# Optimization experiments

Hardware: AMD Instinct MI355X
Metric: run time of the kernel (lower is better)

## Reference

```python
import jax, jax.numpy as jnp
import numpy as np

B, L, DIN, DQ, DS, DP = 16, 2048, 1024, 128, 64, 32

def _lin(k, din, dout):
    k1, k2 = jax.random.split(k)
    s = 1.0 / np.sqrt(din)
    W = jax.random.uniform(k1, (din, dout), jnp.float32, -s, s)
    b = jax.random.uniform(k2, (dout,), jnp.float32, -s, s)
    return W, b

def setup_inputs() -> dict:
    key = jax.random.key(0)
    ks = jax.random.split(key, 13)
    Wq, bq = _lin(ks[0], DIN, DQ)
    Wk, bk = _lin(ks[1], DIN, DQ)
    Wv, bv = _lin(ks[2], DIN, DQ)
    W1, b1 = _lin(ks[3], DS + DP, 128)
    W2, b2 = _lin(ks[4], 128, DQ)
    Wqc, bqc = _lin(ks[5], DQ, DQ)
    Wkc, bkc = _lin(ks[6], DQ, DQ)
    return dict(
        query=jax.random.normal(ks[7], (B, L, DIN), jnp.float32),
        key=jax.random.normal(ks[8], (B, L, DIN), jnp.float32),
        value=jax.random.normal(ks[9], (B, L, DIN), jnp.float32),
        sf=jax.random.normal(ks[10], (B, DS), jnp.float32),
        pos=jax.random.normal(ks[11], (L, DP), jnp.float32),
        Wq=Wq, bq=bq, Wk=Wk, bk=bk, Wv=Wv, bv=bv,
        W1=W1, b1=b1, W2=W2, b2=b2,
        Wqc=Wqc, bqc=bqc, Wkc=Wkc, bkc=bkc,
    )

def reference(query, key, value, sf, pos,
              Wq, bq, Wk, bk, Wv, bv,
              W1, b1, W2, b2, Wqc, bqc, Wkc, bkc):
    b, l, _ = query.shape
    q = query @ Wq + bq            # [b, l, dq]
    k = key @ Wk + bk              # [b, l, dq]
    v = value @ Wv + bv            # [b, l, dq]
    # CPE bias branch (pos is not None)
    sf_exp = jnp.broadcast_to(sf[:, None, :], (b, l, sf.shape[1]))
    pos_exp = jnp.broadcast_to(pos[None, :, :], (b, l, pos.shape[1]))
    cpe = jnp.concatenate([sf_exp, pos_exp], axis=2)         # [b, l, ds+32]
    cpe = jax.nn.relu(cpe @ W1 + b1) @ W2 + b2               # [b, l, dq]
    qc = cpe @ Wqc + bqc
    kc = cpe @ Wkc + bkc
    bias = jnp.einsum('bld,bmd->blm', qc, kc)                # [b, l, l]
    # add_mode == 0: post-softmax additive bias
    scale = jnp.sqrt(jnp.asarray(q.shape[-1], q.dtype))
    scores = jnp.einsum('bld,bmd->blm', q, k) / scale
    attn = jax.nn.softmax(scores, axis=-1) + bias
    out = jnp.einsum('blm,bmd->bld', attn, v)
    # L1 diff-norm regularizer over bias (use_cls=False)
    norm3 = (jnp.sum(jnp.abs(bias[:, 1:, :] - bias[:, :-1, :])) +
             jnp.sum(jnp.abs(bias[:, :, 1:] - bias[:, :, :-1])))
    return out, norm3
```

## Files before the change

### kernel.cpp

```cpp
#include <hip/hip_runtime.h>
#include <hip/hip_bf16.h>

typedef __attribute__((ext_vector_type(8))) short short8;
typedef __attribute__((ext_vector_type(4))) short short4x;
typedef __attribute__((ext_vector_type(4))) float floatx4;

#define MFMA16(a,b,c) __builtin_amdgcn_mfma_f32_16x16x32_bf16((a),(b),(c),0,0,0)

__device__ __forceinline__ unsigned short f2bf(float f) {
  unsigned int x = __float_as_uint(f);
  return (unsigned short)((x + 0x7fffu + ((x >> 16) & 1u)) >> 16);
}
__device__ __forceinline__ float bf2f(unsigned short s) {
  return __uint_as_float(((unsigned int)s) << 16);
}
__device__ __forceinline__ unsigned short f2bf_cvt(float f) {
  unsigned int r;
  asm("v_cvt_pk_bf16_f32 %0, %1, %1" : "=v"(r) : "v"(f));
  return (unsigned short)r;
}

__global__ __launch_bounds__(256)
void prep_kernel(const float* __restrict__ Wq, const float* __restrict__ Wk,
                 const float* __restrict__ Wv, const float* __restrict__ W1,
                 const float* __restrict__ b1, const float* __restrict__ W2,
                 const float* __restrict__ b2, const float* __restrict__ Wqc,
                 const float* __restrict__ bqc, const float* __restrict__ Wkc,
                 const float* __restrict__ bkc, const float* __restrict__ sf,
                 const float* __restrict__ pos,
                 unsigned short* __restrict__ Wf, unsigned short* __restrict__ Ut,
                 float* __restrict__ cqck, float* __restrict__ Asf,
                 float* __restrict__ Ppos)
{
  int blk = blockIdx.x, t = threadIdx.x;
  if (blk < 24) {
    int mat = blk >> 3, cg = blk & 7;
    const float* W = (mat == 0) ? Wq : (mat == 1) ? Wk : Wv;
    int l = t & 63, jp = t >> 6;
    int col = cg * 16 + (l & 15);
    unsigned short* o = Wf + (size_t)mat * 131072 + (size_t)cg * 32 * 512 + l * 8 + jp * 2;
    for (int ks = 0; ks < 32; ++ks) {
      int k = ks * 32 + (l >> 4) * 8 + jp * 2;
      o[ks * 512 + 0] = f2bf(W[(size_t)k * 128 + col]);
      o[ks * 512 + 1] = f2bf(W[(size_t)(k + 1) * 128 + col]);
    }
  } else if (blk >= 384 && blk < 512) {
    int j = blk - 384;
    int k = t & 127;
    const float* Wc = (t < 128) ? Wqc : Wkc;
    float acc = 0.f;
    for (int h = 0; h < 128; ++h) acc += W2[k * 128 + h] * Wc[h * 128 + j];
    Ut[(size_t)((t < 128) ? j : 128 + j) * 128 + k] = f2bf(acc);
  } else if (blk == 512) {
    int j = t & 127;
    const float* Wc = (t < 128) ? Wqc : Wkc;
    const float* bc = (t < 128) ? bqc : bkc;
    float acc = bc[j];
    for (int k = 0; k < 128; ++k) acc += b2[k] * Wc[k * 128 + j];
    cqck[t] = acc;
  } else if (blk > 512 && blk < 529) {
    int b = blk - 513;
    if (t < 128) {
      float acc = 0.f;
      for (int i = 0; i < 64; ++i) acc += sf[b * 64 + i] * W1[i * 128 + t];
      Asf[b * 128 + t] = acc;
    }
  } else if (blk >= 529) {
    int l = blk - 529;
    if (t < 128) {
      float acc = b1[t];
      for (int i = 0; i < 32; ++i) acc += pos[l * 32 + i] * W1[(64 + i) * 128 + t];
      Ppos[l * 128 + t] = acc;
    }
  }
}

__global__ __launch_bounds__(256)
void proj_kernel(const float* __restrict__ X, const unsigned short* __restrict__ Wf,
                 const float* __restrict__ bias,
                 unsigned short* __restrict__ qo, unsigned short* __restrict__ ko,
                 unsigned short* __restrict__ vto, int which)
{
  __shared__ __align__(16) unsigned short X_lds[32 * 1032];

  int t = threadIdx.x;
  int w = t >> 6, l = t & 63;
  int rowbase = blockIdx.x * 32;
  const int lrow = l & 15, hi = l >> 4;
  const float RS2 = 0.08838834764831845f * 1.4426950408889634f;

#pragma unroll
  for (int r = 0; r < 8; ++r) {
    int row = w * 8 + r;
    const float* src = X + (size_t)(rowbase + row) * 1024 + l * 4;
    unsigned short* dst = &X_lds[row * 1032 + l * 4];
#pragma unroll
    for (int i = 0; i < 4; ++i) {
      float4 v = *(const float4*)(src + i * 256);
      short4x s;
      s[0] = (short)f2bf(v.x); s[1] = (short)f2bf(v.y);
      s[2] = (short)f2bf(v.z); s[3] = (short)f2bf(v.w);
      *(short4x*)(dst + i * 256) = s;
    }
  }
  __syncthreads();

  const unsigned short* wp0 = Wf + (size_t)(w * 2) * 32 * 512 + l * 8;
  const unsigned short* wp1 = Wf + (size_t)(w * 2 + 1) * 32 * 512 + l * 8;
  const int xo0 = lrow * 1032 + hi * 8;
  const int xo1 = (lrow + 16) * 1032 + hi * 8;

  floatx4 acc[2][2];
#pragma unroll
  for (int i = 0; i < 2; ++i)
#pragma unroll
    for (int j = 0; j < 2; ++j) { acc[i][j][0]=0.f; acc[i][j][1]=0.f; acc[i][j][2]=0.f; acc[i][j][3]=0.f; }

#pragma unroll 4
  for (int ks = 0; ks < 32; ++ks) {
    short8 b0 = *(const short8*)(wp0 + ks * 512);
    short8 b1 = *(const short8*)(wp1 + ks * 512);
    short8 a0 = *(const short8*)&X_lds[xo0 + ks * 32];
    short8 a1 = *(const short8*)&X_lds[xo1 + ks * 32];
    acc[0][0] = MFMA16(a0, b0, acc[0][0]);
    acc[0][1] = MFMA16(a0, b1, acc[0][1]);
    acc[1][0] = MFMA16(a1, b0, acc[1][0]);
    acc[1][1] = MFMA16(a1, b1, acc[1][1]);
  }

#pragma unroll
  for (int mf = 0; mf < 2; ++mf)
#pragma unroll
    for (int nf = 0; nf < 2; ++nf) {
      int col = w * 32 + nf * 16 + lrow;
      float bb = bias[col];
#pragma unroll
      for (int j = 0; j < 4; ++j) {
        int grow = rowbase + mf * 16 + hi * 4 + j;
        float v = acc[mf][nf][j] + bb;
        if (which == 0) qo[(size_t)grow * 128 + col] = f2bf(v * RS2);
        else if (which == 1) ko[(size_t)grow * 128 + col] = f2bf(v);
        else {
          int b = grow >> 11, li = grow & 2047;
          vto[((size_t)b * 128 + col) * 2048 + li] = f2bf(v);
        }
      }
    }
}

__global__ __launch_bounds__(256)
void qckc_kernel(const float* __restrict__ Asf, const float* __restrict__ Ppos,
                 const unsigned short* __restrict__ Ut, const float* __restrict__ cqck,
                 unsigned short* __restrict__ qc, unsigned short* __restrict__ kc)
{
  __shared__ __align__(16) unsigned short hid[64 * 136];
  int t = threadIdx.x, w = t >> 6, l = t & 63;
  int lbase = blockIdx.x * 64;
  int b = lbase >> 11;
  const int lrow = l & 15, lk = (l >> 4) * 8;
  {
    int r = t >> 2, seg = (t & 3) * 32;
    const float* pp = Ppos + (size_t)((lbase + r) & 2047) * 128 + seg;
    const float* aa = Asf + b * 128 + seg;
    unsigned short* dst = hid + r * 136 + seg;
#pragma unroll
    for (int c = 0; c < 32; c += 4) {
      float4 p4 = *(const float4*)(pp + c);
      float4 a4 = *(const float4*)(aa + c);
      dst[c + 0] = f2bf(fmaxf(p4.x + a4.x, 0.f));
      dst[c + 1] = f2bf(fmaxf(p4.y + a4.y, 0.f));
      dst[c + 2] = f2bf(fmaxf(p4.z + a4.z, 0.f));
      dst[c + 3] = f2bf(fmaxf(p4.w + a4.w, 0.f));
    }
  }
  __syncthreads();
  short8 a[4];
#pragma unroll
  for (int ks = 0; ks < 4; ++ks)
    a[ks] = *(const short8*)&hid[(w * 16 + lrow) * 136 + ks * 32 + lk];
  floatx4 acc[16];
#pragma unroll
  for (int nf = 0; nf < 16; ++nf) { acc[nf][0]=0.f; acc[nf][1]=0.f; acc[nf][2]=0.f; acc[nf][3]=0.f; }
#pragma unroll
  for (int nf = 0; nf < 16; ++nf)
#pragma unroll
    for (int ks = 0; ks < 4; ++ks) {
      short8 bfr = *(const short8*)(Ut + (size_t)(nf * 16 + lrow) * 128 + ks * 32 + lk);
      acc[nf] = MFMA16(a[ks], bfr, acc[nf]);
    }
#pragma unroll
  for (int nf = 0; nf < 16; ++nf) {
    int col = nf * 16 + lrow;
    float bb = cqck[col];
#pragma unroll
    for (int j = 0; j < 4; ++j) {
      int grow = lbase + w * 16 + (l >> 4) * 4 + j;
      float v = acc[nf][j] + bb;
      if (col < 128) qc[(size_t)grow * 128 + col] = f2bf(v);
      else kc[(size_t)grow * 128 + (col - 128)] = f2bf(v);
    }
  }
}

__global__ __launch_bounds__(256)
void m2_partial_kernel(const unsigned short* __restrict__ vt,
                       const unsigned short* __restrict__ kc,
                       float* __restrict__ M2p)
{
  __shared__ __align__(16) unsigned short kct[128 * 40];
  int ks = blockIdx.x, b = blockIdx.y;
  int t = threadIdx.x, w = t >> 6, l = t & 63;
  const int lrow = l & 15, lk = (l >> 4) * 8;
  floatx4 acc[2][8];
#pragma unroll
  for (int i = 0; i < 2; ++i)
#pragma unroll
    for (int j = 0; j < 8; ++j) { acc[i][j][0]=0.f; acc[i][j][1]=0.f; acc[i][j][2]=0.f; acc[i][j][3]=0.f; }
  for (int mc = 0; mc < 8; ++mc) {
    int mbase = ks * 256 + mc * 32;
    {
      int mm = t & 31, ib = (t >> 5) * 16;
      const unsigned short* src = kc + ((size_t)b * 2048 + mbase + mm) * 128 + ib;
#pragma unroll
      for (int ii = 0; ii < 16; ++ii) kct[(ib + ii) * 40 + mm] = src[ii];
    }
    __syncthreads();
#pragma unroll
    for (int mf = 0; mf < 2; ++mf) {
      int jrow = w * 32 + mf * 16 + lrow;
      short8 a = *(const short8*)(vt + ((size_t)b * 128 + jrow) * 2048 + mbase + lk);
#pragma unroll
      for (int nf = 0; nf < 8; ++nf) {
        short8 bfr = *(const short8*)&kct[(nf * 16 + lrow) * 40 + lk];
        acc[mf][nf] = MFMA16(a, bfr, acc[mf][nf]);
      }
    }
    __syncthreads();
  }
#pragma unroll
  for (int mf = 0; mf < 2; ++mf)
#pragma unroll
    for (int nf = 0; nf < 8; ++nf)
#pragma unroll
      for (int j = 0; j < 4; ++j) {
        int jr = w * 32 + mf * 16 + (l >> 4) * 4 + j;
        int ic = nf * 16 + lrow;
        M2p[(((size_t)ks * 16 + b) * 128 + jr) * 128 + ic] = acc[mf][nf][j];
      }
}

__global__ void m2_reduce_kernel(const float* __restrict__ M2p, float* __restrict__ M2t)
{
  int idx = blockIdx.x * 256 + threadIdx.x;
  float s = 0.f;
#pragma unroll
  for (int ksp = 0; ksp < 8; ++ksp) s += M2p[(size_t)ksp * 262144 + idx];
  M2t[idx] = s;
}

__global__ __launch_bounds__(256)
void attn_kernel(const unsigned short* __restrict__ qbf, const unsigned short* __restrict__ kbf,
                 const unsigned short* __restrict__ vt, const unsigned short* __restrict__ qc,
                 const float* __restrict__ M2t, float* __restrict__ out)
{
  __shared__ __align__(16) unsigned short K_lds[64 * 136];
  __shared__ __align__(16) unsigned short V_lds[128 * 72];
  __shared__ __align__(16) unsigned short P_lds[4 * 16 * 72];
  int t = threadIdx.x, w = t >> 6, l = t & 63;
  int lbase = blockIdx.x * 64, b = blockIdx.y;
  const int lrow = l & 15, lk = (l >> 4) * 8;

  size_t browq = (size_t)b * 2048 + lbase + w * 16 + lrow;
  short8 aq[4];
#pragma unroll
  for (int ks = 0; ks < 4; ++ks)
    aq[ks] = *(const short8*)(qbf + browq * 128 + ks * 32 + lk);

  float m_run[4] = {-1e30f, -1e30f, -1e30f, -1e30f};
  float s_run[4] = {0.f, 0.f, 0.f, 0.f};
  floatx4 o[8];
#pragma unroll
  for (int nf = 0; nf < 8; ++nf) { o[nf][0]=0.f; o[nf][1]=0.f; o[nf][2]=0.f; o[nf][3]=0.f; }

  int sr = t >> 2, sseg = (t & 3) * 32;
  int vr = t >> 1, vseg = (t & 1) * 32;

  const short8* ksrc0 = (const short8*)(kbf + ((size_t)b * 2048 + sr) * 128 + sseg);
  const short8* vsrc0 = (const short8*)(vt + ((size_t)b * 128 + vr) * 2048 + vseg);

  short8 kr[4], vrg[4];
#pragma unroll
  for (int i = 0; i < 4; ++i) { kr[i] = ksrc0[i]; vrg[i] = vsrc0[i]; }

  for (int kt = 0; kt < 32; ++kt) {
    {
      short8* dst = (short8*)&K_lds[sr * 136 + sseg];
      dst[0] = kr[0]; dst[1] = kr[1]; dst[2] = kr[2]; dst[3] = kr[3];
      short8* vdst = (short8*)&V_lds[vr * 72 + vseg];
      vdst[0] = vrg[0]; vdst[1] = vrg[1]; vdst[2] = vrg[2]; vdst[3] = vrg[3];
    }
    __syncthreads();
    if (kt < 31) {
      const short8* ks2 = ksrc0 + (size_t)(kt + 1) * 1024;
      const short8* vs2 = vsrc0 + (size_t)(kt + 1) * 8;
#pragma unroll
      for (int i = 0; i < 4; ++i) { kr[i] = ks2[i]; vrg[i] = vs2[i]; }
    }
    floatx4 s[4];
    __builtin_amdgcn_s_setprio(1);
#pragma unroll
    for (int cf = 0; cf < 4; ++cf) {
      floatx4 a4; a4[0]=0.f; a4[1]=0.f; a4[2]=0.f; a4[3]=0.f;
#pragma unroll
      for (int ks = 0; ks < 4; ++ks) {
        short8 bfr = *(const short8*)&K_lds[(cf * 16 + lrow) * 136 + ks * 32 + lk];
        a4 = MFMA16(aq[ks], bfr, a4);
      }
      s[cf] = a4;
    }
    __builtin_amdgcn_s_setprio(0);
    float tm[4];
#pragma unroll
    for (int j = 0; j < 4; ++j) {
      float m0 = fmaxf(fmaxf(s[0][j], s[1][j]), fmaxf(s[2][j], s[3][j]));
#pragma unroll
      for (int off = 1; off < 16; off <<= 1) m0 = fmaxf(m0, __shfl_xor(m0, off, 64));
      tm[j] = m0;
    }
    bool need = (tm[0] > m_run[0] + 8.f) | (tm[1] > m_run[1] + 8.f) |
                (tm[2] > m_run[2] + 8.f) | (tm[3] > m_run[3] + 8.f);
    if (__any(need)) {
      float fmul[4];
#pragma unroll
      for (int j = 0; j < 4; ++j) {
        float nm = fmaxf(m_run[j], tm[j]);
        fmul[j] = exp2f(m_run[j] - nm);
        m_run[j] = nm;
        s_run[j] *= fmul[j];
      }
#pragma unroll
      for (int nf = 0; nf < 8; ++nf)
#pragma unroll
        for (int j = 0; j < 4; ++j) o[nf][j] *= fmul[j];
    }
#pragma unroll
    for (int j = 0; j < 4; ++j) {
      float rs = 0.f;
#pragma unroll
      for (int cf = 0; cf < 4; ++cf) {
        float p = exp2f(s[cf][j] - m_run[j]);
        s[cf][j] = p;
        rs += p;
      }
#pragma unroll
      for (int off = 1; off < 16; off <<= 1) rs += __shfl_xor(rs, off, 64);
      s_run[j] += rs;
    }
    unsigned short* pw = P_lds + w * (16 * 72);
#pragma unroll
    for (int cf = 0; cf < 4; ++cf)
#pragma unroll
      for (int j = 0; j < 4; ++j)
        pw[((l >> 4) * 4 + j) * 72 + cf * 16 + lrow] = f2bf_cvt(s[cf][j]);
    __builtin_amdgcn_s_setprio(1);
#pragma unroll
    for (int kf = 0; kf < 2; ++kf) {
      short8 ap = *(const short8*)&pw[lrow * 72 + kf * 32 + lk];
#pragma unroll
      for (int nf = 0; nf < 8; ++nf) {
        short8 bv = *(const short8*)&V_lds[(nf * 16 + lrow) * 72 + kf * 32 + lk];
        o[nf] = MFMA16(ap, bv, o[nf]);
      }
    }
    __builtin_amdgcn_s_setprio(0);
    __syncthreads();
  }
  float inv[4];
#pragma unroll
  for (int j = 0; j < 4; ++j) inv[j] = 1.f / s_run[j];
#pragma unroll
  for (int nf = 0; nf < 8; ++nf)
#pragma unroll
    for (int j = 0; j < 4; ++j) o[nf][j] *= inv[j];
#pragma unroll
  for (int ks = 0; ks < 4; ++ks) {
    short8 aqc = *(const short8*)(qc + browq * 128 + ks * 32 + lk);
#pragma unroll
    for (int nf = 0; nf < 8; ++nf) {
      const float* mp = M2t + ((size_t)b * 128 + nf * 16 + lrow) * 128 + ks * 32 + lk;
      float4 m0 = *(const float4*)(mp);
      float4 m1 = *(const float4*)(mp + 4);
      short8 bm;
      bm[0]=(short)f2bf(m0.x); bm[1]=(short)f2bf(m0.y); bm[2]=(short)f2bf(m0.z); bm[3]=(short)f2bf(m0.w);
      bm[4]=(short)f2bf(m1.x); bm[5]=(short)f2bf(m1.y); bm[6]=(short)f2bf(m1.z); bm[7]=(short)f2bf(m1.w);
      o[nf] = MFMA16(aqc, bm, o[nf]);
    }
  }
#pragma unroll
  for (int nf = 0; nf < 8; ++nf)
#pragma unroll
    for (int j = 0; j < 4; ++j) {
      int grow = lbase + w * 16 + (l >> 4) * 4 + j;
      out[((size_t)b * 2048 + grow) * 128 + nf * 16 + lrow] = o[nf][j];
    }
}

__global__ __launch_bounds__(256)
void norm_kernel(const unsigned short* __restrict__ qc, const unsigned short* __restrict__ kc,
                 float* __restrict__ partial)
{
  __shared__ __align__(16) unsigned short T1[129 * 136];
  __shared__ __align__(16) unsigned short T2[129 * 136];
  __shared__ float red[8];
  int t = threadIdx.x, w = t >> 6, l = t & 63;
  int ltm = blockIdx.x;
  int lt = ltm >> 4, mt = ltm & 15;
  int b = blockIdx.y;
  const int lrow = l & 15, lk = (l >> 4) * 8;
  {
    int r = t >> 1, half = (t & 1) * 64;
    const unsigned short* asrc = qc + ((size_t)b * 2048 + lt * 128 + r) * 128 + half;
    const unsigned short* bsrc = kc + ((size_t)b * 2048 + mt * 128 + r) * 128 + half;
    unsigned short* adst = T1 + r * 136 + half;
    unsigned short* bdst = T2 + r * 136 + half;
#pragma unroll
    for (int c = 0; c < 64; c += 8) {
      *(short8*)(adst + c) = *(const short8*)(asrc + c);
      *(short8*)(bdst + c) = *(const short8*)(bsrc + c);
    }
    if (t < 16) {
      int gr = lt * 128 + 128; if (gr > 2047) gr = 2047;
      *(short8*)(T1 + 128 * 136 + t * 8) =
          *(const short8*)(qc + ((size_t)b * 2048 + gr) * 128 + t * 8);
    } else if (t < 32) {
      int c = (t - 16) * 8;
      int gr = mt * 128 + 128; if (gr > 2047) gr = 2047;
      *(short8*)(T2 + 128 * 136 + c) =
          *(const short8*)(kc + ((size_t)b * 2048 + gr) * 128 + c);
    }
  }
  __syncthreads();
  floatx4 acc0[2][8], acc1[2][8];
#pragma unroll
  for (int i = 0; i < 2; ++i)
#pragma unroll
    for (int j = 0; j < 8; ++j) {
      acc0[i][j][0]=0.f; acc0[i][j][1]=0.f; acc0[i][j][2]=0.f; acc0[i][j][3]=0.f;
      acc1[i][j][0]=0.f; acc1[i][j][1]=0.f; acc1[i][j][2]=0.f; acc1[i][j][3]=0.f;
    }
#pragma unroll
  for (int ks = 0; ks < 4; ++ks) {
    int off = ks * 32 + lk;
    short8 ad[2], cd[2];
#pragma unroll
    for (int mf = 0; mf < 2; ++mf) {
      int r = w * 32 + mf * 16 + lrow;
      short8 x1 = *(const short8*)&T1[r * 136 + off];
      short8 y1 = *(const short8*)&T1[(r + 1) * 136 + off];
      short8 x2 = *(const short8*)&T2[r * 136 + off];
      short8 y2 = *(const short8*)&T2[(r + 1) * 136 + off];
      short8 d1, d2;
#pragma unroll
      for (int ii = 0; ii < 8; ++ii) {
        d1[ii] = (short)f2bf(bf2f((unsigned short)y1[ii]) - bf2f((unsigned short)x1[ii]));
        d2[ii] = (short)f2bf(bf2f((unsigned short)y2[ii]) - bf2f((unsigned short)x2[ii]));
      }
      ad[mf] = d1; cd[mf] = d2;
    }
#pragma unroll
    for (int nf = 0; nf < 8; ++nf) {
      short8 bk = *(const short8*)&T2[(nf * 16 + lrow) * 136 + off];
      short8 bq = *(const short8*)&T1[(nf * 16 + lrow) * 136 + off];
      acc0[0][nf] = MFMA16(ad[0], bk, acc0[0][nf]);
      acc0[1][nf] = MFMA16(ad[1], bk, acc0[1][nf]);
      acc1[0][nf] = MFMA16(cd[0], bq, acc1[0][nf]);
      acc1[1][nf] = MFMA16(cd[1], bq, acc1[1][nf]);
    }
  }
  float s0 = 0.f, s1 = 0.f;
#pragma unroll
  for (int i = 0; i < 2; ++i)
#pragma unroll
    for (int nf = 0; nf < 8; ++nf)
#pragma unroll
      for (int j = 0; j < 4; ++j) {
        s0 += fabsf(acc0[i][nf][j]);
        s1 += fabsf(acc1[i][nf][j]);
      }
#pragma unroll
  for (int off = 1; off < 64; off <<= 1) {
    s0 += __shfl_xor(s0, off, 64);
    s1 += __shfl_xor(s1, off, 64);
  }
  if (l == 0) { red[w] = s0; red[4 + w] = s1; }
  __syncthreads();
  if (t == 0) {
    partial[((size_t)0 * 16 + b) * 256 + ltm] = red[0] + red[1] + red[2] + red[3];
    partial[((size_t)1 * 16 + b) * 256 + ltm] = red[4] + red[5] + red[6] + red[7];
  }
}

__global__ void norm_reduce_kernel(const float* __restrict__ partial, float* __restrict__ outp)
{
  __shared__ float red[4];
  int t = threadIdx.x;
  float s = 0.f;
  for (int i = t; i < 8192; i += 256) s += partial[i];
#pragma unroll
  for (int off = 1; off < 64; off <<= 1) s += __shfl_xor(s, off, 64);
  if ((t & 63) == 0) red[t >> 6] = s;
  __syncthreads();
  if (t == 0) outp[0] = red[0] + red[1] + red[2] + red[3];
}

extern "C" void kernel_launch(void* const* d_in, const int* in_sizes, int n_in,
                              void* d_out, int out_size, void* d_ws, size_t ws_size,
                              hipStream_t stream)
{
  const float* query = (const float*)d_in[0];
  const float* key_  = (const float*)d_in[1];
  const float* value = (const float*)d_in[2];
  const float* sf    = (const float*)d_in[3];
  const float* pos   = (const float*)d_in[4];
  const float* Wq  = (const float*)d_in[5];  const float* bq  = (const float*)d_in[6];
  const float* Wk  = (const float*)d_in[7];  const float* bk  = (const float*)d_in[8];
  const float* Wv  = (const float*)d_in[9];  const float* bv  = (const float*)d_in[10];
  const float* W1  = (const float*)d_in[11]; const float* b1  = (const float*)d_in[12];
  const float* W2  = (const float*)d_in[13]; const float* b2  = (const float*)d_in[14];
  const float* Wqc = (const float*)d_in[15]; const float* bqc = (const float*)d_in[16];
  const float* Wkc = (const float*)d_in[17]; const float* bkc = (const float*)d_in[18];
  float* out = (float*)d_out;

  char* ws = (char*)d_ws;
  size_t off = 0;
  auto alloc = [&](size_t bytes) {
    char* p = ws + off;
    off += (bytes + 255) & ~(size_t)255;
    return p;
  };
  unsigned short* Wf   = (unsigned short*)alloc((size_t)3 * 131072 * 2);
  unsigned short* Ut   = (unsigned short*)alloc((size_t)256 * 128 * 2);
  float* cqck          = (float*)alloc(256 * 4);
  float* Asf           = (float*)alloc(16 * 128 * 4);
  float* Ppos          = (float*)alloc((size_t)2048 * 128 * 4);
  unsigned short* qbf  = (unsigned short*)alloc((size_t)32768 * 128 * 2);
  unsigned short* kbf  = (unsigned short*)alloc((size_t)32768 * 128 * 2);
  unsigned short* vt   = (unsigned short*)alloc((size_t)32768 * 128 * 2);
  unsigned short* qc   = (unsigned short*)alloc((size_t)32768 * 128 * 2);
  unsigned short* kc   = (unsigned short*)alloc((size_t)32768 * 128 * 2);
  float* M2p           = (float*)alloc((size_t)8 * 262144 * 4);
  float* M2t           = (float*)alloc((size_t)262144 * 4);
  float* npartial      = (float*)alloc((size_t)8192 * 4);
  (void)ws_size; (void)in_sizes; (void)n_in; (void)out_size;

  prep_kernel<<<2577, 256, 0, stream>>>(Wq, Wk, Wv, W1, b1, W2, b2, Wqc, bqc, Wkc, bkc,
                                        sf, pos, Wf, Ut, cqck, Asf, Ppos);
  proj_kernel<<<1024, 256, 0, stream>>>(query, Wf,          bq, qbf, kbf, vt, 0);
  proj_kernel<<<1024, 256, 0, stream>>>(key_,  Wf + 131072, bk, qbf, kbf, vt, 1);
  proj_kernel<<<1024, 256, 0, stream>>>(value, Wf + 262144, bv, qbf, kbf, vt, 2);
  qckc_kernel<<<512, 256, 0, stream>>>(Asf, Ppos, Ut, cqck, qc, kc);
  m2_partial_kernel<<<dim3(8, 16), 256, 0, stream>>>(vt, kc, M2p);
  m2_reduce_kernel<<<1024, 256, 0, stream>>>(M2p, M2t);
  attn_kernel<<<dim3(32, 16), 256, 0, stream>>>(qbf, kbf, vt, qc, M2t, out);
  norm_kernel<<<dim3(256, 16), 256, 0, stream>>>(qc, kc, npartial);
  norm_reduce_kernel<<<1, 256, 0, stream>>>(npartial, out + (size_t)4194304);
}
```

Baseline: 358.9 us.

## Split attention over key halves with a merge kernel; async-load projection inputs

The attention kernel now splits the key/value range into two halves along a third grid dimension, so twice as many blocks run. Each block writes unnormalised partial outputs plus running max and sum, and a new merge kernel combines them flash-decoding style before applying the bias term. The projection kernel now loads fp32 rows straight to LDS with global_load_lds, converts them to bf16 in registers with packed cvt, and uses 16-row tiles, doubling the number of blocks. The split adds about 33 MB of fp32 partial-output traffic and an extra launch in exchange for better occupancy. The projection tile now holds fp32 in LDS and converts on every load rather than once.

```diff
diff --git a/kernel.cpp b/kernel.cpp
--- a/kernel.cpp
+++ b/kernel.cpp
@@ -18,6 +18,20 @@
   unsigned int r;
   asm("v_cvt_pk_bf16_f32 %0, %1, %1" : "=v"(r) : "v"(f));
   return (unsigned short)r;
+}
+__device__ __forceinline__ short8 pack8(float4 f0, float4 f1) {
+  union { unsigned int u[4]; short8 s; } r;
+  asm("v_cvt_pk_bf16_f32 %0, %1, %2" : "=v"(r.u[0]) : "v"(f0.x), "v"(f0.y));
+  asm("v_cvt_pk_bf16_f32 %0, %1, %2" : "=v"(r.u[1]) : "v"(f0.z), "v"(f0.w));
+  asm("v_cvt_pk_bf16_f32 %0, %1, %2" : "=v"(r.u[2]) : "v"(f1.x), "v"(f1.y));
+  asm("v_cvt_pk_bf16_f32 %0, %1, %2" : "=v"(r.u[3]) : "v"(f1.z), "v"(f1.w));
+  return r.s;
+}
+
+typedef const __attribute__((address_space(1))) void* gas_ptr;
+typedef __attribute__((address_space(3))) void* las_ptr;
+__device__ __forceinline__ void gload_lds16(const void* g, void* s) {
+  __builtin_amdgcn_global_load_lds((gas_ptr)g, (las_ptr)s, 16, 0, 0);
 }
 
 __global__ __launch_bounds__(256)
@@ -81,71 +95,57 @@
                  unsigned short* __restrict__ qo, unsigned short* __restrict__ ko,
                  unsigned short* __restrict__ vto, int which)
 {
-  __shared__ __align__(16) unsigned short X_lds[32 * 1032];
-
-  int t = threadIdx.x;
-  int w = t >> 6, l = t & 63;
-  int rowbase = blockIdx.x * 32;
+  __shared__ __align__(16) float X_lds[16 * 1028];
+
+  int t = threadIdx.x, w = t >> 6, l = t & 63;
+  int rowbase = blockIdx.x * 16;
   const int lrow = l & 15, hi = l >> 4;
   const float RS2 = 0.08838834764831845f * 1.4426950408889634f;
 
 #pragma unroll
-  for (int r = 0; r < 8; ++r) {
-    int row = w * 8 + r;
-    const float* src = X + (size_t)(rowbase + row) * 1024 + l * 4;
-    unsigned short* dst = &X_lds[row * 1032 + l * 4];
-#pragma unroll
-    for (int i = 0; i < 4; ++i) {
-      float4 v = *(const float4*)(src + i * 256);
-      short4x s;
-      s[0] = (short)f2bf(v.x); s[1] = (short)f2bf(v.y);
-      s[2] = (short)f2bf(v.z); s[3] = (short)f2bf(v.w);
-      *(short4x*)(dst + i * 256) = s;
-    }
+  for (int i = 0; i < 16; ++i) {
+    int row = w * 4 + (i >> 2), seg = i & 3;
+    gload_lds16(X + (size_t)(rowbase + row) * 1024 + seg * 256 + l * 4,
+                (char*)X_lds + (size_t)row * 4112 + seg * 1024);
   }
   __syncthreads();
 
   const unsigned short* wp0 = Wf + (size_t)(w * 2) * 32 * 512 + l * 8;
   const unsigned short* wp1 = Wf + (size_t)(w * 2 + 1) * 32 * 512 + l * 8;
-  const int xo0 = lrow * 1032 + hi * 8;
-  const int xo1 = (lrow + 16) * 1032 + hi * 8;
-
-  floatx4 acc[2][2];
-#pragma unroll
-  for (int i = 0; i < 2; ++i)
-#pragma unroll
-    for (int j = 0; j < 2; ++j) { acc[i][j][0]=0.f; acc[i][j][1]=0.f; acc[i][j][2]=0.f; acc[i][j][3]=0.f; }
+  const float* ap = &X_lds[lrow * 1028 + hi * 8];
+
+  floatx4 acc0, acc1;
+  acc0[0]=0.f; acc0[1]=0.f; acc0[2]=0.f; acc0[3]=0.f;
+  acc1[0]=0.f; acc1[1]=0.f; acc1[2]=0.f; acc1[3]=0.f;
 
 #pragma unroll 4
   for (int ks = 0; ks < 32; ++ks) {
     short8 b0 = *(const short8*)(wp0 + ks * 512);
     short8 b1 = *(const short8*)(wp1 + ks * 512);
-    short8 a0 = *(const short8*)&X_lds[xo0 + ks * 32];
-    short8 a1 = *(const short8*)&X_lds[xo1 + ks * 32];
-    acc[0][0] = MFMA16(a0, b0, acc[0][0]);
-    acc[0][1] = MFMA16(a0, b1, acc[0][1]);
-    acc[1][0] = MFMA16(a1, b0, acc[1][0]);
-    acc[1][1] = MFMA16(a1, b1, acc[1][1]);
-  }
-
-#pragma unroll
-  for (int mf = 0; mf < 2; ++mf)
-#pragma unroll
-    for (int nf = 0; nf < 2; ++nf) {
-      int col = w * 32 + nf * 16 + lrow;
-      float bb = bias[col];
-#pragma unroll
-      for (int j = 0; j < 4; ++j) {
-        int grow = rowbase + mf * 16 + hi * 4 + j;
-        float v = acc[mf][nf][j] + bb;
-        if (which == 0) qo[(size_t)grow * 128 + col] = f2bf(v * RS2);
-        else if (which == 1) ko[(size_t)grow * 128 + col] = f2bf(v);
-        else {
-          int b = grow >> 11, li = grow & 2047;
-          vto[((size_t)b * 128 + col) * 2048 + li] = f2bf(v);
-        }
-      }
-    }
+    float4 f0 = *(const float4*)(ap + ks * 32);
+    float4 f1 = *(const float4*)(ap + ks * 32 + 4);
+    short8 a = pack8(f0, f1);
+    acc0 = MFMA16(a, b0, acc0);
+    acc1 = MFMA16(a, b1, acc1);
+  }
+
+#pragma unroll
+  for (int nf = 0; nf < 2; ++nf) {
+    int col = w * 32 + nf * 16 + lrow;
+    float bb = bias[col];
+    floatx4 av = (nf == 0) ? acc0 : acc1;
+#pragma unroll
+    for (int j = 0; j < 4; ++j) {
+      int grow = rowbase + hi * 4 + j;
+      float v = av[j] + bb;
+      if (which == 0) qo[(size_t)grow * 128 + col] = f2bf(v * RS2);
+      else if (which == 1) ko[(size_t)grow * 128 + col] = f2bf(v);
+      else {
+        int b = grow >> 11, li = grow & 2047;
+        vto[((size_t)b * 128 + col) * 2048 + li] = f2bf(v);
+      }
+    }
+  }
 }
 
 __global__ __launch_bounds__(256)
@@ -259,15 +259,16 @@
 }
 
 __global__ __launch_bounds__(256)
-void attn_kernel(const unsigned short* __restrict__ qbf, const unsigned short* __restrict__ kbf,
-                 const unsigned short* __restrict__ vt, const unsigned short* __restrict__ qc,
-                 const float* __restrict__ M2t, float* __restrict__ out)
+void attn_partial_kernel(const unsigned short* __restrict__ qbf,
+                         const unsigned short* __restrict__ kbf,
+                         const unsigned short* __restrict__ vt,
+                         float* __restrict__ op, float* __restrict__ ms)
 {
   __shared__ __align__(16) unsigned short K_lds[64 * 136];
   __shared__ __align__(16) unsigned short V_lds[128 * 72];
   __shared__ __align__(16) unsigned short P_lds[4 * 16 * 72];
   int t = threadIdx.x, w = t >> 6, l = t & 63;
-  int lbase = blockIdx.x * 64, b = blockIdx.y;
+  int lbase = blockIdx.x * 64, b = blockIdx.y, z = blockIdx.z;
   const int lrow = l & 15, lk = (l >> 4) * 8;
 
   size_t browq = (size_t)b * 2048 + lbase + w * 16 + lrow;
@@ -285,14 +286,14 @@
   int sr = t >> 2, sseg = (t & 3) * 32;
   int vr = t >> 1, vseg = (t & 1) * 32;
 
-  const short8* ksrc0 = (const short8*)(kbf + ((size_t)b * 2048 + sr) * 128 + sseg);
-  const short8* vsrc0 = (const short8*)(vt + ((size_t)b * 128 + vr) * 2048 + vseg);
+  const short8* ksrc0 = (const short8*)(kbf + ((size_t)b * 2048 + z * 1024 + sr) * 128 + sseg);
+  const short8* vsrc0 = (const short8*)(vt + ((size_t)b * 128 + vr) * 2048 + z * 1024 + vseg);
 
   short8 kr[4], vrg[4];
 #pragma unroll
   for (int i = 0; i < 4; ++i) { kr[i] = ksrc0[i]; vrg[i] = vsrc0[i]; }
 
-  for (int kt = 0; kt < 32; ++kt) {
+  for (int kt = 0; kt < 16; ++kt) {
     {
       short8* dst = (short8*)&K_lds[sr * 136 + sseg];
       dst[0] = kr[0]; dst[1] = kr[1]; dst[2] = kr[2]; dst[3] = kr[3];
@@ -300,7 +301,7 @@
       vdst[0] = vrg[0]; vdst[1] = vrg[1]; vdst[2] = vrg[2]; vdst[3] = vrg[3];
     }
     __syncthreads();
-    if (kt < 31) {
+    if (kt < 15) {
       const short8* ks2 = ksrc0 + (size_t)(kt + 1) * 1024;
       const short8* vs2 = vsrc0 + (size_t)(kt + 1) * 8;
 #pragma unroll
@@ -375,13 +376,59 @@
     __builtin_amdgcn_s_setprio(0);
     __syncthreads();
   }
-  float inv[4];
-#pragma unroll
-  for (int j = 0; j < 4; ++j) inv[j] = 1.f / s_run[j];
+  size_t obase = (size_t)(z * 16 + b) * 2048;
 #pragma unroll
   for (int nf = 0; nf < 8; ++nf)
 #pragma unroll
-    for (int j = 0; j < 4; ++j) o[nf][j] *= inv[j];
+    for (int j = 0; j < 4; ++j) {
+      int grow = lbase + w * 16 + (l >> 4) * 4 + j;
+      op[(obase + grow) * 128 + nf * 16 + lrow] = o[nf][j];
+    }
+  if (lrow == 0) {
+#pragma unroll
+    for (int j = 0; j < 4; ++j) {
+      int row = lbase + w * 16 + (l >> 4) * 4 + j;
+      ms[(obase + row) * 2 + 0] = m_run[j];
+      ms[(obase + row) * 2 + 1] = s_run[j];
+    }
+  }
+}
+
+__global__ __launch_bounds__(256)
+void attn_merge_kernel(const float* __restrict__ op, const float* __restrict__ ms,
+                       const unsigned short* __restrict__ qc,
+                       const float* __restrict__ M2t, float* __restrict__ out)
+{
+  int t = threadIdx.x, w = t >> 6, l = t & 63;
+  int lbase = blockIdx.x * 64, b = blockIdx.y;
+  const int lrow = l & 15, lk = (l >> 4) * 8;
+  size_t browq = (size_t)b * 2048 + lbase + w * 16 + lrow;
+
+  float f0[4], f1[4], inv[4];
+#pragma unroll
+  for (int j = 0; j < 4; ++j) {
+    int row = lbase + w * 16 + (l >> 4) * 4 + j;
+    float m0 = ms[((size_t)(b) * 2048 + row) * 2 + 0];
+    float s0 = ms[((size_t)(b) * 2048 + row) * 2 + 1];
+    float m1 = ms[((size_t)(16 + b) * 2048 + row) * 2 + 0];
+    float s1 = ms[((size_t)(16 + b) * 2048 + row) * 2 + 1];
+    float M = fmaxf(m0, m1);
+    f0[j] = exp2f(m0 - M);
+    f1[j] = exp2f(m1 - M);
+    inv[j] = 1.f / (s0 * f0[j] + s1 * f1[j]);
+  }
+  floatx4 o[8];
+#pragma unroll
+  for (int nf = 0; nf < 8; ++nf) {
+    int col = nf * 16 + lrow;
+#pragma unroll
+    for (int j = 0; j < 4; ++j) {
+      int grow = lbase + w * 16 + (l >> 4) * 4 + j;
+      float o0 = op[((size_t)(b) * 2048 + grow) * 128 + col];
+      float o1 = op[((size_t)(16 + b) * 2048 + grow) * 128 + col];
+      o[nf][j] = (o0 * f0[j] + o1 * f1[j]) * inv[j];
+    }
+  }
 #pragma unroll
   for (int ks = 0; ks < 4; ++ks) {
     short8 aqc = *(const short8*)(qc + browq * 128 + ks * 32 + lk);
@@ -390,9 +437,7 @@
       const float* mp = M2t + ((size_t)b * 128 + nf * 16 + lrow) * 128 + ks * 32 + lk;
       float4 m0 = *(const float4*)(mp);
       float4 m1 = *(const float4*)(mp + 4);
-      short8 bm;
-      bm[0]=(short)f2bf(m0.x); bm[1]=(short)f2bf(m0.y); bm[2]=(short)f2bf(m0.z); bm[3]=(short)f2bf(m0.w);
-      bm[4]=(short)f2bf(m1.x); bm[5]=(short)f2bf(m1.y); bm[6]=(short)f2bf(m1.z); bm[7]=(short)f2bf(m1.w);
+      short8 bm = pack8(m0, m1);
       o[nf] = MFMA16(aqc, bm, o[nf]);
     }
   }
@@ -551,17 +596,20 @@
   float* M2p           = (float*)alloc((size_t)8 * 262144 * 4);
   float* M2t           = (float*)alloc((size_t)262144 * 4);
   float* npartial      = (float*)alloc((size_t)8192 * 4);
+  float* op            = (float*)alloc((size_t)32 * 2048 * 128 * 4);
+  float* ms            = (float*)alloc((size_t)32 * 2048 * 2 * 4);
   (void)ws_size; (void)in_sizes; (void)n_in; (void)out_size;
 
   prep_kernel<<<2577, 256, 0, stream>>>(Wq, Wk, Wv, W1, b1, W2, b2, Wqc, bqc, Wkc, bkc,
                                         sf, pos, Wf, Ut, cqck, Asf, Ppos);
-  proj_kernel<<<1024, 256, 0, stream>>>(query, Wf,          bq, qbf, kbf, vt, 0);
-  proj_kernel<<<1024, 256, 0, stream>>>(key_,  Wf + 131072, bk, qbf, kbf, vt, 1);
-  proj_kernel<<<1024, 256, 0, stream>>>(value, Wf + 262144, bv, qbf, kbf, vt, 2);
+  proj_kernel<<<2048, 256, 0, stream>>>(query, Wf,          bq, qbf, kbf, vt, 0);
+  proj_kernel<<<2048, 256, 0, stream>>>(key_,  Wf + 131072, bk, qbf, kbf, vt, 1);
+  proj_kernel<<<2048, 256, 0, stream>>>(value, Wf + 262144, bv, qbf, kbf, vt, 2);
   qckc_kernel<<<512, 256, 0, stream>>>(Asf, Ppos, Ut, cqck, qc, kc);
   m2_partial_kernel<<<dim3(8, 16), 256, 0, stream>>>(vt, kc, M2p);
   m2_reduce_kernel<<<1024, 256, 0, stream>>>(M2p, M2t);
-  attn_kernel<<<dim3(32, 16), 256, 0, stream>>>(qbf, kbf, vt, qc, M2t, out);
+  attn_partial_kernel<<<dim3(32, 16, 2), 256, 0, stream>>>(qbf, kbf, vt, op, ms);
+  attn_merge_kernel<<<dim3(32, 16), 256, 0, stream>>>(op, ms, qc, M2t, out);
   norm_kernel<<<dim3(256, 16), 256, 0, stream>>>(qc, kc, npartial);
   norm_reduce_kernel<<<1, 256, 0, stream>>>(npartial, out + (size_t)4194304);
 }
```

Measured after the change: 371.0 us. 1.03x slower.
